# Optimization experiments

Hardware: AMD Instinct MI355X
Metric: run time of the kernel (lower is better)

The kernel has to match this reference:

```python
import jax, jax.numpy as jnp
import numpy as np

B, S, D, H = 2, 2048, 1024, 16
DK = D // H


def setup_inputs() -> dict:
    key = jax.random.key(0)
    ks = jax.random.split(key, 9)
    sc = 0.02
    return {
        "x": jax.random.normal(ks[0], (B, S, D), dtype=jnp.float32),
        "attention_mask": jnp.ones((B, S), dtype=jnp.int32),
        "Wq": jax.random.normal(ks[1], (D, D), dtype=jnp.float32) * sc,
        "bq": jax.random.normal(ks[2], (D,), dtype=jnp.float32) * sc,
        "Wk": jax.random.normal(ks[3], (D, D), dtype=jnp.float32) * sc,
        "bk": jax.random.normal(ks[4], (D,), dtype=jnp.float32) * sc,
        "Wv": jax.random.normal(ks[5], (D, D), dtype=jnp.float32) * sc,
        "bv": jax.random.normal(ks[6], (D,), dtype=jnp.float32) * sc,
        "Wo": jax.random.normal(ks[7], (D, D), dtype=jnp.float32) * sc,
        "bo": jax.random.normal(ks[8], (D,), dtype=jnp.float32) * sc,
    }


def reference(x, attention_mask, Wq, bq, Wk, bk, Wv, bv, Wo, bo):
    b, s, d = x.shape
    # projections (Linear: x @ W + b) then split heads -> [b, h, s, dk]
    def heads(t):
        return t.reshape(b, s, H, DK).transpose(0, 2, 1, 3)
    Q = heads(x @ Wq + bq)
    K = heads(x @ Wk + bk)
    V = heads(x @ Wv + bv)
    # NOTE: original computes K @ Q^T (not Q @ K^T) and applies NO 1/sqrt(dk) scale
    scores = jnp.einsum("bhid,bhjd->bhij", K, Q)  # [b, h, s, s]
    causal = jnp.tril(jnp.ones((s, s), dtype=bool))  # [s, s]
    final_mask = attention_mask[:, None, None, :].astype(bool) & causal[None, None]
    scores = jnp.where(final_mask, scores, -jnp.inf)
    attn = jax.nn.softmax(scores, axis=-1)
    out = jnp.einsum("bhij,bhjd->bhid", attn, V)  # [b, h, s, dk]
    out = out.transpose(0, 2, 1, 3).reshape(b, s, d)
    return out @ Wo + bo
```

## Files before the change

### kernel.cpp

```cpp
#include <hip/hip_runtime.h>
#include <stdint.h>
#include <stddef.h>


typedef short bf16x8 __attribute__((ext_vector_type(8)));
typedef float f32x4  __attribute__((ext_vector_type(4)));

__device__ __forceinline__ short f2bf(float f) {
  union { float f; uint32_t u; } a; a.f = f;
  uint32_t r = a.u + 0x7fffu + ((a.u >> 16) & 1u);
  return (short)(r >> 16);
}
__device__ __forceinline__ float bf2f(short s) {
  union { uint32_t u; float f; } a; a.u = ((uint32_t)(uint16_t)s) << 16;
  return a.f;
}
__device__ __forceinline__ uint32_t pack2bf(float a, float b) {
  union { float f; uint32_t u; } x, y; x.f = a; y.f = b;
  return (x.u >> 16) | (y.u & 0xffff0000u);
}
__device__ __forceinline__ float fast_exp2(float x) {
#if __has_builtin(__builtin_amdgcn_exp2f)
  return __builtin_amdgcn_exp2f(x);
#else
  return exp2f(x);
#endif
}
__device__ __forceinline__ void async16(const void* g, void* l) {
  __builtin_amdgcn_global_load_lds(
      (const __attribute__((address_space(1))) uint32_t*)g,
      (__attribute__((address_space(3))) uint32_t*)l, 16, 0, 0);
}
#define MFMA(a, b, c) __builtin_amdgcn_mfma_f32_16x16x32_bf16((a), (b), (c), 0, 0, 0)

__global__ void k_split_x(const float* __restrict__ x, short* __restrict__ xhi,
                          short* __restrict__ xlo) {
  int i = blockIdx.x * 256 + threadIdx.x;
  float4 v = ((const float4*)x)[i];
  short4 h, l;
  h.x = f2bf(v.x); l.x = f2bf(v.x - bf2f(h.x));
  h.y = f2bf(v.y); l.y = f2bf(v.y - bf2f(h.y));
  h.z = f2bf(v.z); l.z = f2bf(v.z - bf2f(h.z));
  h.w = f2bf(v.w); l.w = f2bf(v.w - bf2f(h.w));
  ((short4*)xhi)[i] = h;
  ((short4*)xlo)[i] = l;
}

__global__ void k_prep_w(const float* __restrict__ Wq, const float* __restrict__ Wk,
                         const float* __restrict__ Wv, const float* __restrict__ Wo,
                         short* __restrict__ whi, short* __restrict__ wo) {
  __shared__ float T[64][65];
  int z = blockIdx.z;
  const float* W = (z == 0) ? Wq : (z == 1) ? Wk : (z == 2) ? Wv : Wo;
  int n0 = blockIdx.x * 64, k0 = blockIdx.y * 64;
  int t = threadIdx.x;
  int rr = t >> 4, cc = (t & 15) * 4;
#pragma unroll
  for (int it = 0; it < 4; ++it) {
    int row = rr + it * 16;
    float4 v = *(const float4*)&W[(size_t)(k0 + row) * 1024 + n0 + cc];
    T[row][cc] = v.x; T[row][cc + 1] = v.y; T[row][cc + 2] = v.z; T[row][cc + 3] = v.w;
  }
  __syncthreads();
  short* oh = (z < 3) ? (whi + (size_t)z * 1048576) : wo;
#pragma unroll
  for (int it = 0; it < 4; ++it) {
    int nrow = rr + it * 16;
    short4 h4;
    h4.x = f2bf(T[cc + 0][nrow]);
    h4.y = f2bf(T[cc + 1][nrow]);
    h4.z = f2bf(T[cc + 2][nrow]);
    h4.w = f2bf(T[cc + 3][nrow]);
    *(short4*)&oh[(size_t)(n0 + nrow) * 1024 + k0 + cc] = h4;
  }
}

__global__ __launch_bounds__(256, 3) void k_gemm_qkv(
    const short* __restrict__ xhi, const short* __restrict__ xlo,
    const short* __restrict__ whi,
    const float* __restrict__ bq, const float* __restrict__ bk,
    const float* __restrict__ bv,
    short* __restrict__ Qhi, short* __restrict__ Qlo,
    short* __restrict__ Khi, short* __restrict__ Klo,
    short* __restrict__ Vt) {
  __shared__ short AH[2][4096];
  __shared__ short AL[2][4096];
  __shared__ short BH[2][4096];
  int tid = threadIdx.x;
  int bx = blockIdx.x;
  int m0 = blockIdx.y * 128;
  int n0g = bx * 128;
  bool SPLIT = (bx < 16);
  int w = tid >> 6, lane = tid & 63, lr = lane & 15, lq = lane >> 4;
  int wm = w >> 1, wn = w & 1;
  f32x4 acc[4][4] = {};

  auto stage = [&](int ks, int pb) {
#pragma unroll
    for (int it = 0; it < 2; ++it) {
      int idx = it * 256 + tid;
      int row = idx >> 2, c = idx & 3;
      int cs = c ^ (row & 3);
      size_t ga = (size_t)(m0 + row) * 1024 + ks * 32 + cs * 8;
      async16(xhi + ga, &AH[pb][idx * 8]);
      if (SPLIT) async16(xlo + ga, &AL[pb][idx * 8]);
      size_t gb = (size_t)(n0g + row) * 1024 + ks * 32 + cs * 8;
      async16(whi + gb, &BH[pb][idx * 8]);
    }
  };

  stage(0, 0);
  int p = 0;
  int g = lq ^ (lr & 3);
  for (int ks = 0; ks < 32; ++ks) {
    __syncthreads();
    if (ks < 31) stage(ks + 1, p ^ 1);
    const bf16x8* A8 = (const bf16x8*)AH[p];
    const bf16x8* L8 = (const bf16x8*)AL[p];
    const bf16x8* B8 = (const bf16x8*)BH[p];
    bf16x8 af[4], al[4], bfr[4];
#pragma unroll
    for (int mt = 0; mt < 4; ++mt) af[mt] = A8[(wm * 64 + mt * 16 + lr) * 4 + g];
#pragma unroll
    for (int nt = 0; nt < 4; ++nt) bfr[nt] = B8[(wn * 64 + nt * 16 + lr) * 4 + g];
    if (SPLIT) {
#pragma unroll
      for (int mt = 0; mt < 4; ++mt) al[mt] = L8[(wm * 64 + mt * 16 + lr) * 4 + g];
    }
#pragma unroll
    for (int mt = 0; mt < 4; ++mt)
#pragma unroll
      for (int nt = 0; nt < 4; ++nt)
        acc[mt][nt] = MFMA(af[mt], bfr[nt], acc[mt][nt]);
    if (SPLIT) {
#pragma unroll
      for (int mt = 0; mt < 4; ++mt)
#pragma unroll
        for (int nt = 0; nt < 4; ++nt)
          acc[mt][nt] = MFMA(al[mt], bfr[nt], acc[mt][nt]);
    }
    p ^= 1;
  }

  int z = bx >> 3;
  const float LOG2E = 1.44269504f;
  if (z == 2) {
#pragma unroll
    for (int nt = 0; nt < 4; ++nt) {
      int dg = (n0g & 1023) + wn * 64 + nt * 16 + lr;
      float bvv = bv[dg];
      int hh = dg >> 6, dk = dg & 63;
#pragma unroll
      for (int mt = 0; mt < 4; ++mt) {
        int row = m0 + wm * 64 + mt * 16 + lq * 4;
        int b_ = row >> 11, s_ = row & 2047;
        short4 pk;
        pk.x = f2bf(acc[mt][nt][0] + bvv);
        pk.y = f2bf(acc[mt][nt][1] + bvv);
        pk.z = f2bf(acc[mt][nt][2] + bvv);
        pk.w = f2bf(acc[mt][nt][3] + bvv);
        *(short4*)&Vt[(size_t)((b_ * 16 + hh) * 64 + dk) * 2048 + s_] = pk;
      }
    }
  } else {
    const float* bias = (z == 0) ? bq : bk;
    short* Ch = (z == 0) ? Qhi : Khi;
    short* Cl = (z == 0) ? Qlo : Klo;
#pragma unroll
    for (int nt = 0; nt < 4; ++nt) {
      int colg = (n0g & 1023) + wn * 64 + nt * 16 + lr;
      float bvv = bias[colg];
#pragma unroll
      for (int mt = 0; mt < 4; ++mt)
#pragma unroll
        for (int r = 0; r < 4; ++r) {
          int row = m0 + wm * 64 + mt * 16 + lq * 4 + r;
          float v = acc[mt][nt][r] + bvv;
          if (z == 0) v *= LOG2E;
          size_t o = (size_t)row * 1024 + colg;
          short hh = f2bf(v);
          Ch[o] = hh;
          Cl[o] = f2bf(v - bf2f(hh));
        }
    }
  }
}

__global__ __launch_bounds__(256, 4) void k_gemm_o(
    const short* __restrict__ Ab, const short* __restrict__ Bb,
    const float* __restrict__ bias, float* __restrict__ Cf) {
  __shared__ short AH[2][4096];
  __shared__ short BH[2][2048];
  int tid = threadIdx.x;
  int m0 = blockIdx.y * 128, n0 = blockIdx.x * 64;
  int w = tid >> 6, lane = tid & 63, lr = lane & 15, lq = lane >> 4;
  f32x4 acc[2][4] = {};

  auto stage = [&](int ks, int pb) {
#pragma unroll
    for (int it = 0; it < 2; ++it) {
      int idx = it * 256 + tid;
      int row = idx >> 2, c = idx & 3;
      int cs = c ^ (row & 3);
      async16(Ab + (size_t)(m0 + row) * 1024 + ks * 32 + cs * 8, &AH[pb][idx * 8]);
    }
    {
      int idx = tid;
      int row = idx >> 2, c = idx & 3;
      int cs = c ^ (row & 3);
      async16(Bb + (size_t)(n0 + row) * 1024 + ks * 32 + cs * 8, &BH[pb][idx * 8]);
    }
  };

  stage(0, 0);
  int p = 0;
  int g = lq ^ (lr & 3);
  for (int ks = 0; ks < 32; ++ks) {
    __syncthreads();
    if (ks < 31) stage(ks + 1, p ^ 1);
    const bf16x8* A8 = (const bf16x8*)AH[p];
    const bf16x8* B8 = (const bf16x8*)BH[p];
    bf16x8 af[2], bfr[4];
#pragma unroll
    for (int mt = 0; mt < 2; ++mt) af[mt] = A8[(w * 32 + mt * 16 + lr) * 4 + g];
#pragma unroll
    for (int nt = 0; nt < 4; ++nt) bfr[nt] = B8[(nt * 16 + lr) * 4 + g];
#pragma unroll
    for (int mt = 0; mt < 2; ++mt)
#pragma unroll
      for (int nt = 0; nt < 4; ++nt)
        acc[mt][nt] = MFMA(af[mt], bfr[nt], acc[mt][nt]);
    p ^= 1;
  }
#pragma unroll
  for (int nt = 0; nt < 4; ++nt) {
    int col = n0 + nt * 16 + lr;
    float bvv = bias[col];
#pragma unroll
    for (int mt = 0; mt < 2; ++mt)
#pragma unroll
      for (int r = 0; r < 4; ++r) {
        int row = m0 + w * 32 + mt * 16 + lq * 4 + r;
        Cf[(size_t)row * 1024 + col] = acc[mt][nt][r] + bvv;
      }
  }
}

__global__ __launch_bounds__(256, 3) void k_attn(
    const short* __restrict__ Khi, const short* __restrict__ Klo,
    const short* __restrict__ Qhi, const short* __restrict__ Qlo,
    const short* __restrict__ Vt, const int* __restrict__ amask,
    short* __restrict__ Obuf) {
  __shared__ short QH[2][4096];
  __shared__ short QL[2][4096];
  __shared__ short VS[2][4096];
  int tid = threadIdx.x;
  int bid = blockIdx.x;
  int xcd = bid & 7, idx = bid >> 3;
  int bh = xcd * 4 + (idx >> 5);
  int L  = 32 - (idx & 31);
  int b = bh >> 4, h = bh & 15;
  int w = tid >> 6, lane = tid & 63, lr = lane & 15, lq = lane >> 4;
  int band = 2 * (L - 1) + (w >> 1);
  int rb0 = band * 32 + (w & 1) * 16;

  bf16x8 kh[2], kl[2];
  {
    size_t ra = ((size_t)(b * 2048 + rb0 + lr)) * 1024 + h * 64;
#pragma unroll
    for (int ks = 0; ks < 2; ++ks) {
      kh[ks] = *(const bf16x8*)(Khi + ra + ks * 32 + lq * 8);
      kl[ks] = *(const bf16x8*)(Klo + ra + ks * 32 + lq * 8);
    }
  }

  f32x4 O[4] = {};
  float ls = 0.f;
  int iq = rb0 + lr;
  int baddr0 = (((lq & 1) * 2) * 16 + lr) * 4;
  int baddr1 = baddr0 + 64;

  auto stage = [&](int jt, int pb) {
    int j0 = jt * 64;
#pragma unroll
    for (int it = 0; it < 2; ++it) {
      int idx2 = it * 256 + tid;
      int rr = idx2 >> 3, c = idx2 & 7;
      int cs = c ^ (rr & 7);
      size_t gq = ((size_t)(b * 2048 + j0 + rr)) * 1024 + h * 64 + cs * 8;
      async16(Qhi + gq, &QH[pb][idx2 * 8]);
      async16(Qlo + gq, &QL[pb][idx2 * 8]);
      size_t gv = ((size_t)(bh * 64 + rr)) * 2048 + j0 + cs * 8;
      async16(Vt + gv, &VS[pb][idx2 * 8]);
    }
  };

  stage(0, 0);
  int p = 0;
  for (int t = 0; t < L; ++t) {
    __syncthreads();
    if (t + 1 < L) stage(t + 1, p ^ 1);
    int j0 = t * 64;
    const bf16x8* Q8 = (const bf16x8*)QH[p];
    const bf16x8* L8 = (const bf16x8*)QL[p];
    const bf16x8* V8 = (const bf16x8*)VS[p];

    int av = amask[b * 2048 + j0 + lane];
    unsigned long long bal = __ballot(av != 0);
    bool allv = (bal == ~0ull);

    f32x4 s[4] = {};
#pragma unroll
    for (int mt = 0; mt < 4; ++mt) {
      int row = mt * 16 + lr;
#pragma unroll
      for (int ks = 0; ks < 2; ++ks) {
        int gi = row * 8 + ((ks * 4 + lq) ^ (row & 7));
        bf16x8 qa = Q8[gi];
        bf16x8 la = L8[gi];
        s[mt] = MFMA(qa, kh[ks], s[mt]);
        s[mt] = MFMA(la, kh[ks], s[mt]);
        s[mt] = MFMA(qa, kl[ks], s[mt]);
      }
    }

    bool diag = (t == L - 1);
    float pv[4][4];
#pragma unroll
    for (int mt = 0; mt < 4; ++mt)
#pragma unroll
      for (int r = 0; r < 4; ++r)
        pv[mt][r] = fast_exp2(s[mt][r]);
    if (diag) {
#pragma unroll
      for (int mt = 0; mt < 4; ++mt)
#pragma unroll
        for (int r = 0; r < 4; ++r)
          if (j0 + mt * 16 + lq * 4 + r > iq) pv[mt][r] = 0.f;
    }
    if (!allv) {
#pragma unroll
      for (int mt = 0; mt < 4; ++mt)
#pragma unroll
        for (int r = 0; r < 4; ++r)
          if (!((bal >> (mt * 16 + lq * 4 + r)) & 1)) pv[mt][r] = 0.f;
    }
    uint32_t pd[4][2];
#pragma unroll
    for (int mt = 0; mt < 4; ++mt) {
      ls += (pv[mt][0] + pv[mt][1]) + (pv[mt][2] + pv[mt][3]);
      pd[mt][0] = pack2bf(pv[mt][0], pv[mt][1]);
      pd[mt][1] = pack2bf(pv[mt][2], pv[mt][3]);
    }

#pragma unroll
    for (int k2 = 0; k2 < 2; ++k2) {
      union { int i[4]; bf16x8 v; } pa;
#pragma unroll
      for (int dd = 0; dd < 4; ++dd) {
        int addr = (dd >> 1) ? baddr1 : baddr0;
        int v0 = __builtin_amdgcn_ds_bpermute(addr, (int)pd[k2 * 2 + 0][dd & 1]);
        int v1 = __builtin_amdgcn_ds_bpermute(addr, (int)pd[k2 * 2 + 1][dd & 1]);
        pa.i[dd] = (lq >> 1) ? v1 : v0;
      }
#pragma unroll
      for (int nt = 0; nt < 4; ++nt) {
        int row = nt * 16 + lr;
        bf16x8 vb = V8[row * 8 + ((k2 * 4 + lq) ^ (row & 7))];
        O[nt] = MFMA(pa.v, vb, O[nt]);
      }
    }
    p ^= 1;
  }

  float tsum = ls;
  tsum += __shfl_xor(tsum, 16);
  tsum += __shfl_xor(tsum, 32);
  float inv[4];
#pragma unroll
  for (int r = 0; r < 4; ++r) inv[r] = 1.0f / __shfl(tsum, lq * 4 + r, 64);
#pragma unroll
  for (int nt = 0; nt < 4; ++nt)
#pragma unroll
    for (int r = 0; r < 4; ++r) {
      int row = b * 2048 + rb0 + lq * 4 + r;
      int col = h * 64 + nt * 16 + lr;
      Obuf[(size_t)row * 1024 + col] = f2bf(O[nt][r] * inv[r]);
    }
}

extern "C" void kernel_launch(void* const* d_in, const int* in_sizes, int n_in,
                              void* d_out, int out_size, void* d_ws, size_t ws_size,
                              hipStream_t stream) {
  const float* x  = (const float*)d_in[0];
  const int* amask = (const int*)d_in[1];
  const float* Wq = (const float*)d_in[2];
  const float* bq = (const float*)d_in[3];
  const float* Wk = (const float*)d_in[4];
  const float* bk = (const float*)d_in[5];
  const float* Wv = (const float*)d_in[6];
  const float* bv = (const float*)d_in[7];
  const float* Wo = (const float*)d_in[8];
  const float* bo = (const float*)d_in[9];

  char* ws = (char*)d_ws;
  const size_t MB = 1024 * 1024;
  short* xhi = (short*)(ws);
  short* xlo = (short*)(ws + 8 * MB);
  short* whi = (short*)(ws + 16 * MB);
  short* wo  = (short*)(ws + 26 * MB);
  short* Qhi = (short*)(ws + 28 * MB);
  short* Qlo = (short*)(ws + 36 * MB);
  short* Khi = (short*)(ws + 44 * MB);
  short* Klo = (short*)(ws + 52 * MB);
  short* Vt  = (short*)(ws + 60 * MB);
  short* Obuf = xhi;

  k_split_x<<<4096, 256, 0, stream>>>(x, xhi, xlo);
  k_prep_w<<<dim3(16, 16, 4), 256, 0, stream>>>(Wq, Wk, Wv, Wo, whi, wo);

  k_gemm_qkv<<<dim3(24, 32), 256, 0, stream>>>(xhi, xlo, whi, bq, bk, bv,
                                               Qhi, Qlo, Khi, Klo, Vt);
  k_attn<<<1024, 256, 0, stream>>>(Khi, Klo, Qhi, Qlo, Vt, amask, Obuf);
  k_gemm_o<<<dim3(16, 32), 256, 0, stream>>>(Obuf, wo, bo, (float*)d_out);
}
```

Baseline: 239.4 us.

## Drop x low-part split in QKV GEMM, shrink O-proj tiles, reorder attention blocks

Removes the hi/lo bf16 split of x, so the Q and K projections use a single bf16 MFMA pass instead of two and the xlo buffer is no longer written or read. The output projection tile shrinks from 128x64 to 64x64 and the grid doubles, giving more blocks and lower per-block LDS. The attention block-to-(head, length) mapping is reordered so that neighbouring blocks interleave heads and long causal bands are scheduled first. The cost is lower precision in Q and K, which feed unscaled softmax scores, so accuracy against the reference may suffer.

```diff
diff --git a/kernel.cpp b/kernel.cpp
--- a/kernel.cpp
+++ b/kernel.cpp
@@ -33,17 +33,15 @@
 }
 #define MFMA(a, b, c) __builtin_amdgcn_mfma_f32_16x16x32_bf16((a), (b), (c), 0, 0, 0)
 
-__global__ void k_split_x(const float* __restrict__ x, short* __restrict__ xhi,
-                          short* __restrict__ xlo) {
+__global__ void k_split_x(const float* __restrict__ x, short* __restrict__ xhi) {
   int i = blockIdx.x * 256 + threadIdx.x;
   float4 v = ((const float4*)x)[i];
-  short4 h, l;
-  h.x = f2bf(v.x); l.x = f2bf(v.x - bf2f(h.x));
-  h.y = f2bf(v.y); l.y = f2bf(v.y - bf2f(h.y));
-  h.z = f2bf(v.z); l.z = f2bf(v.z - bf2f(h.z));
-  h.w = f2bf(v.w); l.w = f2bf(v.w - bf2f(h.w));
+  short4 h;
+  h.x = f2bf(v.x);
+  h.y = f2bf(v.y);
+  h.z = f2bf(v.z);
+  h.w = f2bf(v.w);
   ((short4*)xhi)[i] = h;
-  ((short4*)xlo)[i] = l;
 }
 
 __global__ void k_prep_w(const float* __restrict__ Wq, const float* __restrict__ Wk,
@@ -76,21 +74,18 @@
 }
 
 __global__ __launch_bounds__(256, 3) void k_gemm_qkv(
-    const short* __restrict__ xhi, const short* __restrict__ xlo,
-    const short* __restrict__ whi,
+    const short* __restrict__ xhi, const short* __restrict__ whi,
     const float* __restrict__ bq, const float* __restrict__ bk,
     const float* __restrict__ bv,
     short* __restrict__ Qhi, short* __restrict__ Qlo,
     short* __restrict__ Khi, short* __restrict__ Klo,
     short* __restrict__ Vt) {
   __shared__ short AH[2][4096];
-  __shared__ short AL[2][4096];
   __shared__ short BH[2][4096];
   int tid = threadIdx.x;
   int bx = blockIdx.x;
   int m0 = blockIdx.y * 128;
   int n0g = bx * 128;
-  bool SPLIT = (bx < 16);
   int w = tid >> 6, lane = tid & 63, lr = lane & 15, lq = lane >> 4;
   int wm = w >> 1, wn = w & 1;
   f32x4 acc[4][4] = {};
@@ -101,11 +96,8 @@
       int idx = it * 256 + tid;
       int row = idx >> 2, c = idx & 3;
       int cs = c ^ (row & 3);
-      size_t ga = (size_t)(m0 + row) * 1024 + ks * 32 + cs * 8;
-      async16(xhi + ga, &AH[pb][idx * 8]);
-      if (SPLIT) async16(xlo + ga, &AL[pb][idx * 8]);
-      size_t gb = (size_t)(n0g + row) * 1024 + ks * 32 + cs * 8;
-      async16(whi + gb, &BH[pb][idx * 8]);
+      async16(xhi + (size_t)(m0 + row) * 1024 + ks * 32 + cs * 8, &AH[pb][idx * 8]);
+      async16(whi + (size_t)(n0g + row) * 1024 + ks * 32 + cs * 8, &BH[pb][idx * 8]);
     }
   };
 
@@ -116,29 +108,17 @@
     __syncthreads();
     if (ks < 31) stage(ks + 1, p ^ 1);
     const bf16x8* A8 = (const bf16x8*)AH[p];
-    const bf16x8* L8 = (const bf16x8*)AL[p];
     const bf16x8* B8 = (const bf16x8*)BH[p];
-    bf16x8 af[4], al[4], bfr[4];
+    bf16x8 af[4], bfr[4];
 #pragma unroll
     for (int mt = 0; mt < 4; ++mt) af[mt] = A8[(wm * 64 + mt * 16 + lr) * 4 + g];
 #pragma unroll
     for (int nt = 0; nt < 4; ++nt) bfr[nt] = B8[(wn * 64 + nt * 16 + lr) * 4 + g];
-    if (SPLIT) {
-#pragma unroll
-      for (int mt = 0; mt < 4; ++mt) al[mt] = L8[(wm * 64 + mt * 16 + lr) * 4 + g];
-    }
 #pragma unroll
     for (int mt = 0; mt < 4; ++mt)
 #pragma unroll
       for (int nt = 0; nt < 4; ++nt)
         acc[mt][nt] = MFMA(af[mt], bfr[nt], acc[mt][nt]);
-    if (SPLIT) {
-#pragma unroll
-      for (int mt = 0; mt < 4; ++mt)
-#pragma unroll
-        for (int nt = 0; nt < 4; ++nt)
-          acc[mt][nt] = MFMA(al[mt], bfr[nt], acc[mt][nt]);
-    }
     p ^= 1;
   }
 
@@ -189,27 +169,18 @@
 __global__ __launch_bounds__(256, 4) void k_gemm_o(
     const short* __restrict__ Ab, const short* __restrict__ Bb,
     const float* __restrict__ bias, float* __restrict__ Cf) {
-  __shared__ short AH[2][4096];
+  __shared__ short AH[2][2048];
   __shared__ short BH[2][2048];
   int tid = threadIdx.x;
-  int m0 = blockIdx.y * 128, n0 = blockIdx.x * 64;
+  int m0 = blockIdx.y * 64, n0 = blockIdx.x * 64;
   int w = tid >> 6, lane = tid & 63, lr = lane & 15, lq = lane >> 4;
-  f32x4 acc[2][4] = {};
+  f32x4 acc[4] = {};
 
   auto stage = [&](int ks, int pb) {
-#pragma unroll
-    for (int it = 0; it < 2; ++it) {
-      int idx = it * 256 + tid;
-      int row = idx >> 2, c = idx & 3;
-      int cs = c ^ (row & 3);
-      async16(Ab + (size_t)(m0 + row) * 1024 + ks * 32 + cs * 8, &AH[pb][idx * 8]);
-    }
-    {
-      int idx = tid;
-      int row = idx >> 2, c = idx & 3;
-      int cs = c ^ (row & 3);
-      async16(Bb + (size_t)(n0 + row) * 1024 + ks * 32 + cs * 8, &BH[pb][idx * 8]);
-    }
+    int row = tid >> 2, c = tid & 3;
+    int cs = c ^ (row & 3);
+    async16(Ab + (size_t)(m0 + row) * 1024 + ks * 32 + cs * 8, &AH[pb][tid * 8]);
+    async16(Bb + (size_t)(n0 + row) * 1024 + ks * 32 + cs * 8, &BH[pb][tid * 8]);
   };
 
   stage(0, 0);
@@ -220,16 +191,13 @@
     if (ks < 31) stage(ks + 1, p ^ 1);
     const bf16x8* A8 = (const bf16x8*)AH[p];
     const bf16x8* B8 = (const bf16x8*)BH[p];
-    bf16x8 af[2], bfr[4];
-#pragma unroll
-    for (int mt = 0; mt < 2; ++mt) af[mt] = A8[(w * 32 + mt * 16 + lr) * 4 + g];
+    bf16x8 af = A8[(w * 16 + lr) * 4 + g];
+    bf16x8 bfr[4];
 #pragma unroll
     for (int nt = 0; nt < 4; ++nt) bfr[nt] = B8[(nt * 16 + lr) * 4 + g];
 #pragma unroll
-    for (int mt = 0; mt < 2; ++mt)
-#pragma unroll
-      for (int nt = 0; nt < 4; ++nt)
-        acc[mt][nt] = MFMA(af[mt], bfr[nt], acc[mt][nt]);
+    for (int nt = 0; nt < 4; ++nt)
+      acc[nt] = MFMA(af, bfr[nt], acc[nt]);
     p ^= 1;
   }
 #pragma unroll
@@ -237,12 +205,10 @@
     int col = n0 + nt * 16 + lr;
     float bvv = bias[col];
 #pragma unroll
-    for (int mt = 0; mt < 2; ++mt)
-#pragma unroll
-      for (int r = 0; r < 4; ++r) {
-        int row = m0 + w * 32 + mt * 16 + lq * 4 + r;
-        Cf[(size_t)row * 1024 + col] = acc[mt][nt][r] + bvv;
-      }
+    for (int r = 0; r < 4; ++r) {
+      int row = m0 + w * 16 + lq * 4 + r;
+      Cf[(size_t)row * 1024 + col] = acc[nt][r] + bvv;
+    }
   }
 }
 
@@ -257,8 +223,8 @@
   int tid = threadIdx.x;
   int bid = blockIdx.x;
   int xcd = bid & 7, idx = bid >> 3;
-  int bh = xcd * 4 + (idx >> 5);
-  int L  = 32 - (idx & 31);
+  int bh = xcd * 4 + (idx & 3);
+  int L  = 32 - (idx >> 2);
   int b = bh >> 4, h = bh & 15;
   int w = tid >> 6, lane = tid & 63, lr = lane & 15, lq = lane >> 4;
   int band = 2 * (L - 1) + (w >> 1);
@@ -406,7 +372,6 @@
   char* ws = (char*)d_ws;
   const size_t MB = 1024 * 1024;
   short* xhi = (short*)(ws);
-  short* xlo = (short*)(ws + 8 * MB);
   short* whi = (short*)(ws + 16 * MB);
   short* wo  = (short*)(ws + 26 * MB);
   short* Qhi = (short*)(ws + 28 * MB);
@@ -416,11 +381,11 @@
   short* Vt  = (short*)(ws + 60 * MB);
   short* Obuf = xhi;
 
-  k_split_x<<<4096, 256, 0, stream>>>(x, xhi, xlo);
+  k_split_x<<<4096, 256, 0, stream>>>(x, xhi);
   k_prep_w<<<dim3(16, 16, 4), 256, 0, stream>>>(Wq, Wk, Wv, Wo, whi, wo);
 
-  k_gemm_qkv<<<dim3(24, 32), 256, 0, stream>>>(xhi, xlo, whi, bq, bk, bv,
+  k_gemm_qkv<<<dim3(24, 32), 256, 0, stream>>>(xhi, whi, bq, bk, bv,
                                                Qhi, Qlo, Khi, Klo, Vt);
   k_attn<<<1024, 256, 0, stream>>>(Khi, Klo, Qhi, Qlo, Vt, amask, Obuf);
-  k_gemm_o<<<dim3(16, 32), 256, 0, stream>>>(Obuf, wo, bo, (float*)d_out);
-}
+  k_gemm_o<<<dim3(16, 64), 256, 0, stream>>>(Obuf, wo, bo, (float*)d_out);
+}
```

New measurement: 210.9 us. 1.14x faster.
